# Kernel optimization log

Hardware: AMD Instinct MI355X
Metric: run time of the kernel (lower is better)

The kernel has to match this reference:

```python
import jax, jax.numpy as jnp
import numpy as np

N_PAPER, N_AUTHOR, E = 100000, 50000, 1000000
D_PAPER, D_AUTHOR, HID, OUT = 256, 128, 256, 349


def setup_inputs() -> dict:
    key = jax.random.key(0)
    ks = jax.random.split(key, 16)
    s = 0.05
    return {
        'x_paper': jax.random.normal(ks[0], (N_PAPER, D_PAPER), jnp.float32),
        'x_author': jax.random.normal(ks[1], (N_AUTHOR, D_AUTHOR), jnp.float32),
        'cites': jax.random.randint(ks[2], (2, E), 0, N_PAPER, jnp.int64 if jax.config.jax_enable_x64 else jnp.int32),
        'writes_src': jax.random.randint(ks[3], (E,), 0, N_AUTHOR),
        'writes_dst': jax.random.randint(ks[4], (E,), 0, N_PAPER),
        'gcn_W1': jax.random.normal(ks[5], (D_PAPER, HID), jnp.float32) * s,
        'gcn_b1': jnp.zeros((HID,), jnp.float32),
        'sage_Wl1': jax.random.normal(ks[6], (D_AUTHOR, HID), jnp.float32) * s,
        'sage_bl1': jnp.zeros((HID,), jnp.float32),
        'sage_Wr1': jax.random.normal(ks[7], (D_PAPER, HID), jnp.float32) * s,
        'gcn_W2': jax.random.normal(ks[8], (HID, HID), jnp.float32) * s,
        'gcn_b2': jnp.zeros((HID,), jnp.float32),
        'sage_Wl2': jax.random.normal(ks[9], (D_AUTHOR, HID), jnp.float32) * s,
        'sage_bl2': jnp.zeros((HID,), jnp.float32),
        'sage_Wr2': jax.random.normal(ks[10], (HID, HID), jnp.float32) * s,
        'lin_W': jax.random.normal(ks[11], (HID, OUT), jnp.float32) * s,
        'lin_b': jnp.zeros((OUT,), jnp.float32),
    }


def _gcn_conv(x, W, b, src, dst, n):
    # GCNConv with add_self_loops=True, symmetric normalization
    loop = jnp.arange(n, dtype=src.dtype)
    si = jnp.concatenate([src, loop])
    di = jnp.concatenate([dst, loop])
    deg = jax.ops.segment_sum(jnp.ones_like(di, x.dtype), di, n)
    dinv = jnp.where(deg > 0, jax.lax.rsqrt(jnp.maximum(deg, 1.0)), 0.0)
    norm = dinv[si] * dinv[di]  # [E+n]
    h = x @ W                   # [n, hid]
    out = jax.ops.segment_sum(h[si] * norm[:, None], di, n)
    return out + b


def _sage_conv(x_src, x_dst, Wl, bl, Wr, src, dst, n_dst):
    # SAGEConv: mean-aggregate neighbors -> lin_l, plus root lin_r (no bias)
    agg = jax.ops.segment_sum(x_src[src], dst, n_dst)
    cnt = jax.ops.segment_sum(jnp.ones_like(dst, x_src.dtype), dst, n_dst)
    mean = agg / jnp.maximum(cnt, 1.0)[:, None]
    return mean @ Wl + bl + x_dst @ Wr


def reference(x_paper, x_author, cites, writes_src, writes_dst,
              gcn_W1, gcn_b1, sage_Wl1, sage_bl1, sage_Wr1,
              gcn_W2, gcn_b2, sage_Wl2, sage_bl2, sage_Wr2,
              lin_W, lin_b):
    n = x_paper.shape[0]
    c_src, c_dst = cites[0], cites[1]
    # layer 1: HeteroConv with aggr='sum' over the two edge-type outputs
    p = jax.nn.relu(
        _gcn_conv(x_paper, gcn_W1, gcn_b1, c_src, c_dst, n)
        + _sage_conv(x_author, x_paper, sage_Wl1, sage_bl1, sage_Wr1, writes_src, writes_dst, n))
    # layer 2 (author features are never updated by these edge types)
    p = jax.nn.relu(
        _gcn_conv(p, gcn_W2, gcn_b2, c_src, c_dst, n)
        + _sage_conv(x_author, p, sage_Wl2, sage_bl2, sage_Wr2, writes_src, writes_dst, n))
    return p @ lin_W + lin_b
```

## Files before the change

### kernel.cpp

```cpp
#include <hip/hip_runtime.h>


#define DP   256
#define DA   128
#define HIDN 256
#define DOUT 349
#define NBKT 782
#define CHUNK 4096

typedef unsigned short u16;
typedef unsigned int u32;
typedef __attribute__((ext_vector_type(8))) short bf16x8;
typedef __attribute__((ext_vector_type(4))) float f32x4;

__device__ __forceinline__ u16 bf16_rn(float x) {
  union { float f; unsigned u; } v; v.f = x;
  unsigned r = v.u + 0x7FFFu + ((v.u >> 16) & 1u);
  return (u16)(r >> 16);
}
__device__ __forceinline__ float bf16f(u16 h) {
  union { float f; unsigned u; } v; v.u = ((unsigned)h) << 16; return v.f;
}
__device__ __forceinline__ unsigned pack2(float a, float b) {
  return (unsigned)bf16_rn(a) | ((unsigned)bf16_rn(b) << 16);
}

__device__ __forceinline__ void gload16(const void* g, void* lds) {
  __builtin_amdgcn_global_load_lds(
      (const __attribute__((address_space(1))) unsigned int*)g,
      (__attribute__((address_space(3))) unsigned int*)lds, 16, 0, 0);
}

#define SCAN_TPB 256
#define SCAN_VPT 8
#define SCAN_TILE 2048

__global__ void scan_local(const int* __restrict__ in, int* __restrict__ out,
                           int* __restrict__ bsum, int n) {
  __shared__ int sdata[SCAN_TPB];
  int t = threadIdx.x;
  int base = blockIdx.x * SCAN_TILE + t * SCAN_VPT;
  int v[SCAN_VPT];
  int sum = 0;
#pragma unroll
  for (int j = 0; j < SCAN_VPT; ++j) {
    int idx = base + j;
    v[j] = (idx < n) ? in[idx] : 0;
    sum += v[j];
  }
  sdata[t] = sum;
  __syncthreads();
  for (int off = 1; off < SCAN_TPB; off <<= 1) {
    int x = (t >= off) ? sdata[t - off] : 0;
    __syncthreads();
    sdata[t] += x;
    __syncthreads();
  }
  int prefix = sdata[t] - sum;
  if (t == SCAN_TPB - 1) bsum[blockIdx.x] = sdata[t];
  int run = prefix;
#pragma unroll
  for (int j = 0; j < SCAN_VPT; ++j) {
    int idx = base + j;
    if (idx < n) out[idx] = run;
    run += v[j];
  }
}

__global__ void scan_spine(int* __restrict__ bsum, int nb) {
  __shared__ int sdata[256];
  int t = threadIdx.x;
  int v = (t < nb) ? bsum[t] : 0;
  sdata[t] = v;
  __syncthreads();
  for (int off = 1; off < 256; off <<= 1) {
    int x = (t >= off) ? sdata[t - off] : 0;
    __syncthreads();
    sdata[t] += x;
    __syncthreads();
  }
  if (t < nb) bsum[t] = sdata[t] - v;
}

__global__ void scan_add(int* __restrict__ out, const int* __restrict__ bsum, int n) {
  int add = bsum[blockIdx.x];
  int base = blockIdx.x * SCAN_TILE + threadIdx.x * SCAN_VPT;
#pragma unroll
  for (int j = 0; j < SCAN_VPT; ++j) {
    int idx = base + j;
    if (idx < n) out[idx] += add;
  }
}

__global__ __launch_bounds__(256) void sort_pass1(
    const int* __restrict__ c_src, const int* __restrict__ c_dst,
    const int* __restrict__ w_srcP, const int* __restrict__ w_dstP,
    u32* __restrict__ tmp, int* __restrict__ gcount, int* __restrict__ lofs,
    int E, int nch) {
  const int cg = blockIdx.x, t = threadIdx.x;
  const int et = cg >= nch;
  const int c = cg - et * nch;
  const int* src = et ? w_srcP : c_src;
  const int* dst = et ? w_dstP : c_dst;
  __shared__ u32 cnt[NBKT];
  __shared__ u32 ofs[NBKT];
  __shared__ u32 sdata[256];
  __shared__ u32 pay[CHUNK];
  __shared__ u16 bkt[CHUNK];

  for (int i = t; i < NBKT; i += 256) cnt[i] = 0;
  __syncthreads();
  const int base = c * CHUNK;
#pragma unroll
  for (int j = 0; j < 16; ++j) {
    int i = t + j * 256, idx = base + i;
    if (idx < E) {
      u32 s = (u32)src[idx], d = (u32)dst[idx];
      pay[i] = (s << 7) | (d & 127u);
      bkt[i] = (u16)(d >> 7);
      atomicAdd(&cnt[d >> 7], 1u);
    }
  }
  __syncthreads();
  for (int i = t; i < NBKT; i += 256)
    gcount[((size_t)et * NBKT + i) * nch + c] = (int)cnt[i];
  u32 ssum = 0;
  const int b0 = t * 4;
#pragma unroll
  for (int j = 0; j < 4; ++j) {
    int i = b0 + j;
    if (i < NBKT) ssum += cnt[i];
  }
  sdata[t] = ssum;
  __syncthreads();
  for (int o = 1; o < 256; o <<= 1) {
    u32 x = (t >= o) ? sdata[t - o] : 0;
    __syncthreads();
    sdata[t] += x;
    __syncthreads();
  }
  u32 run = sdata[t] - ssum;
#pragma unroll
  for (int j = 0; j < 4; ++j) {
    int i = b0 + j;
    if (i < NBKT) { ofs[i] = run; run += cnt[i]; }
  }
  __syncthreads();
  for (int i = t; i < NBKT; i += 256) {
    lofs[((size_t)et * nch + c) * NBKT + i] = (int)ofs[i];
    cnt[i] = ofs[i];
  }
  __syncthreads();
  u32* tout = tmp + (size_t)et * nch * CHUNK + base;
#pragma unroll
  for (int j = 0; j < 16; ++j) {
    int i = t + j * 256, idx = base + i;
    if (idx < E) {
      u32 p = atomicAdd(&cnt[bkt[i]], 1u);
      tout[p] = pay[i];
    }
  }
}

#define MAXB 2560
__global__ __launch_bounds__(256) void sort_pass2(
    const u32* __restrict__ tmp, const int* __restrict__ prefix,
    const int* __restrict__ gcount, const int* __restrict__ lofs,
    int* __restrict__ cSorted, int* __restrict__ cDeg, int* __restrict__ cOff,
    int* __restrict__ wSorted, int* __restrict__ wDeg, int* __restrict__ wOff,
    float* __restrict__ dinv,
    int E, int nch, int n, int nbk) {
  const int bg = blockIdx.x, t = threadIdx.x;
  const int et = bg >= nbk;
  const int b = bg - et * nbk;
  int* outSorted = et ? wSorted : cSorted;
  int* deg = et ? wDeg : cDeg;
  int* offArr = et ? wOff : cOff;
  __shared__ u32 est[MAXB];
  __shared__ u32 outl[MAXB];
  __shared__ u32 cnt[128], ofs[128];
  __shared__ u32 sdata[256];

  const int node0 = b << 7;
  const size_t bgl = (size_t)et * NBKT + b;
  const int ebaseG = prefix[bgl * nch];
  const int eendG = (bg == 2 * nbk - 1) ? 2 * E : prefix[(bgl + 1) * nch];
  const int ebase = ebaseG - et * E;
  const int esize = (eendG - et * E) - ebase;

  const u32* tsrc = tmp + (size_t)et * nch * CHUNK;
  for (int c = t; c < nch; c += 256) {
    int g = lofs[((size_t)et * nch + c) * NBKT + b];
    int len = gcount[bgl * nch + c];
    int dp = prefix[bgl * nch + c] - ebaseG;
    for (int k = 0; k < len; ++k)
      est[dp + k] = tsrc[(size_t)c * CHUNK + g + k];
  }
  if (t < 128) cnt[t] = 0;
  __syncthreads();
  for (int i = t; i < esize; i += 256) atomicAdd(&cnt[est[i] & 127u], 1u);
  __syncthreads();
  u32 v = (t < 128) ? cnt[t] : 0;
  sdata[t] = v;
  __syncthreads();
  for (int o = 1; o < 256; o <<= 1) {
    u32 x = (t >= o) ? sdata[t - o] : 0;
    __syncthreads();
    sdata[t] += x;
    __syncthreads();
  }
  if (t < 128) ofs[t] = sdata[t] - v;
  __syncthreads();
  const int nNodes = (n - node0) < 128 ? (n - node0) : 128;
  if (t < nNodes) {
    deg[node0 + t] = (int)cnt[t];
    offArr[node0 + t] = ebase + (int)ofs[t];
    if (et == 0) dinv[node0 + t] = rsqrtf((float)(cnt[t] + 1));
  }
  __syncthreads();
  if (t < 128) cnt[t] = ofs[t];
  __syncthreads();
  for (int i = t; i < esize; i += 256) {
    u32 e = est[i];
    u32 p = atomicAdd(&cnt[e & 127u], 1u);
    outl[p] = e >> 7;
  }
  __syncthreads();
  for (int i = t; i < esize; i += 256) outSorted[ebase + i] = (int)outl[i];
}

__global__ void prep_all(
    const float* __restrict__ x_paper, const float* __restrict__ x_author,
    u16* __restrict__ xp, u16* __restrict__ xa16,
    const float* __restrict__ W1, const float* __restrict__ Wr1,
    const float* __restrict__ W2, const float* __restrict__ Wr2,
    const float* __restrict__ Wl1, const float* __restrict__ Wl2,
    const float* __restrict__ linW,
    u16* __restrict__ BtW1, u16* __restrict__ BtWr1,
    u16* __restrict__ BtW2, u16* __restrict__ BtWr2,
    u16* __restrict__ BtWl1, u16* __restrict__ BtWl2, u16* __restrict__ BtLin,
    const float* __restrict__ b1, const float* __restrict__ bl1,
    const float* __restrict__ b2, const float* __restrict__ bl2,
    const float* __restrict__ linb,
    float* __restrict__ biasR1, float* __restrict__ biasR2,
    float* __restrict__ biasLin,
    int N, int NA) {
  const int R1 = (N * 32 + 255) / 256;
  const int R2 = R1 + (NA * 16 + 255) / 256;
  const int WB = 256 * 256 / 256;
  const int LB = 256 * 128 / 256;
  const int FB = 384 * 256 / 256;
  int bid = blockIdx.x, t = threadIdx.x;

  if (bid < R1) {
    int i = bid * 256 + t;
    if (i < N * 32) {
      const float4* x4 = (const float4*)x_paper;
      float4 v0 = x4[(size_t)i * 2];
      float4 v1 = x4[(size_t)i * 2 + 1];
      uint4 O;
      O.x = pack2(v0.x, v0.y); O.y = pack2(v0.z, v0.w);
      O.z = pack2(v1.x, v1.y); O.w = pack2(v1.z, v1.w);
      ((uint4*)xp)[i] = O;
    }
    return;
  }
  if (bid < R2) {
    int i = (bid - R1) * 256 + t;
    if (i < NA * 16) {
      const float4* x4 = (const float4*)x_author;
      float4 v0 = x4[(size_t)i * 2];
      float4 v1 = x4[(size_t)i * 2 + 1];
      uint4 O;
      O.x = pack2(v0.x, v0.y); O.y = pack2(v0.z, v0.w);
      O.z = pack2(v1.x, v1.y); O.w = pack2(v1.z, v1.w);
      ((uint4*)xa16)[i] = O;
    }
    return;
  }
  int wb = bid - R2;
  const float* W; u16* Bt; int K, Nn, Npad;
  if      (wb < WB)                  { W = W1;  Bt = BtW1;  K = 256; Nn = 256; Npad = 256; }
  else if ((wb -= WB) < WB)          { W = Wr1; Bt = BtWr1; K = 256; Nn = 256; Npad = 256; }
  else if ((wb -= WB) < WB)          { W = W2;  Bt = BtW2;  K = 256; Nn = 256; Npad = 256; }
  else if ((wb -= WB) < WB)          { W = Wr2; Bt = BtWr2; K = 256; Nn = 256; Npad = 256; }
  else if ((wb -= WB) < LB)          { W = Wl1; Bt = BtWl1; K = 128; Nn = 256; Npad = 256; }
  else if ((wb -= LB) < LB)          { W = Wl2; Bt = BtWl2; K = 128; Nn = 256; Npad = 256; }
  else if ((wb -= LB) < FB)          { W = linW; Bt = BtLin; K = 256; Nn = DOUT; Npad = 384; }
  else {
    if (t < 256) {
      biasR1[t] = b1[t] + bl1[t];
      biasR2[t] = b2[t] + bl2[t];
    }
    for (int i = t; i < 384; i += 256) biasLin[i] = (i < DOUT) ? linb[i] : 0.f;
    return;
  }
  int idx = wb * 256 + t;
  int tot = Npad * K;
  if (idx >= tot) return;
  int nn = idx / K, k = idx - nn * K;
  float v = (nn < Nn) ? W[(size_t)k * Nn + nn] : 0.f;
  Bt[idx] = bf16_rn(v);
}

__device__ __forceinline__ void agg_body(
    const uint4* __restrict__ base, const float* __restrict__ dinv,
    const int* __restrict__ c_off, const int* __restrict__ c_cnt,
    const int* __restrict__ c_sorted, u16* __restrict__ xout,
    int d, int lane) {
  const int hl = lane & 31;
  const int half = lane >> 5;
  int start = c_off[d], cnt = c_cnt[d];
  float acc[8] = {};
  for (int j0 = 0; j0 < cnt; j0 += 64) {
    int nn = cnt - j0; nn = nn < 64 ? nn : 64;
    int sl = (j0 + lane < cnt) ? c_sorted[start + j0 + lane] : 0;
    int jj = 0;
    for (; jj + 8 <= nn; jj += 8) {
      int ss[4]; float dv[4]; uint4 vv[4];
#pragma unroll
      for (int u = 0; u < 4; ++u) ss[u] = __shfl(sl, jj + 2 * u + half);
#pragma unroll
      for (int u = 0; u < 4; ++u) dv[u] = dinv[ss[u]];
#pragma unroll
      for (int u = 0; u < 4; ++u) vv[u] = base[(size_t)ss[u] * 32 + hl];
#pragma unroll
      for (int u = 0; u < 4; ++u) {
        const u16* p = (const u16*)&vv[u];
#pragma unroll
        for (int e = 0; e < 8; ++e) acc[e] = fmaf(bf16f(p[e]), dv[u], acc[e]);
      }
    }
    for (; jj < nn; jj += 2) {
      int idx = jj + half;
      int s = __shfl(sl, idx < nn ? idx : jj);
      float wgt = (idx < nn) ? dinv[s] : 0.f;
      uint4 v = base[(size_t)s * 32 + hl];
      const u16* p = (const u16*)&v;
#pragma unroll
      for (int e = 0; e < 8; ++e) acc[e] = fmaf(bf16f(p[e]), wgt, acc[e]);
    }
  }
  float dd = dinv[d];
  {
    uint4 v = base[(size_t)d * 32 + hl];
    float wgt = half ? 0.f : dd;
    const u16* p = (const u16*)&v;
#pragma unroll
    for (int e = 0; e < 8; ++e) acc[e] = fmaf(bf16f(p[e]), wgt, acc[e]);
  }
  float f[8];
#pragma unroll
  for (int e = 0; e < 8; ++e) f[e] = (acc[e] + __shfl_xor(acc[e], 32)) * dd;
  if (lane < 32) {
    uint4 O;
    O.x = pack2(f[0], f[1]); O.y = pack2(f[2], f[3]);
    O.z = pack2(f[4], f[5]); O.w = pack2(f[6], f[7]);
    ((uint4*)xout)[(size_t)d * 32 + hl] = O;
  }
}

__device__ __forceinline__ void mean_body(
    const uint4* __restrict__ xa, const int* __restrict__ w_off,
    const int* __restrict__ w_cnt, const int* __restrict__ w_sorted,
    u16* __restrict__ mean, int d, int lane) {
  const int hl = lane & 15;
  const int qt = lane >> 4;
  int start = w_off[d], cnt = w_cnt[d];
  float acc[8] = {};
  for (int j0 = 0; j0 < cnt; j0 += 64) {
    int nn = cnt - j0; nn = nn < 64 ? nn : 64;
    int sl = (j0 + lane < cnt) ? w_sorted[start + j0 + lane] : 0;
    int jj = 0;
    for (; jj + 8 <= nn; jj += 8) {
      int ss[2]; uint4 vv[2];
#pragma unroll
      for (int u = 0; u < 2; ++u) ss[u] = __shfl(sl, jj + 4 * u + qt);
#pragma unroll
      for (int u = 0; u < 2; ++u) vv[u] = xa[(size_t)ss[u] * 16 + hl];
#pragma unroll
      for (int u = 0; u < 2; ++u) {
        const u16* p = (const u16*)&vv[u];
#pragma unroll
        for (int e = 0; e < 8; ++e) acc[e] += bf16f(p[e]);
      }
    }
    for (; jj < nn; jj += 4) {
      int idx = jj + qt;
      int s = __shfl(sl, idx < nn ? idx : jj);
      float wgt = (idx < nn) ? 1.f : 0.f;
      uint4 v = xa[(size_t)s * 16 + hl];
      const u16* p = (const u16*)&v;
#pragma unroll
      for (int e = 0; e < 8; ++e) acc[e] = fmaf(bf16f(p[e]), wgt, acc[e]);
    }
  }
  float inv = 1.0f / (float)((cnt > 0) ? cnt : 1);
  float f[8];
#pragma unroll
  for (int e = 0; e < 8; ++e) {
    float x = acc[e] + __shfl_xor(acc[e], 16);
    x += __shfl_xor(x, 32);
    f[e] = x * inv;
  }
  if (lane < 16) {
    uint4 O;
    O.x = pack2(f[0], f[1]); O.y = pack2(f[2], f[3]);
    O.z = pack2(f[4], f[5]); O.w = pack2(f[6], f[7]);
    ((uint4*)mean)[(size_t)d * 16 + hl] = O;
  }
}

__global__ void gather_fused(
    const u16* __restrict__ xin, const float* __restrict__ dinv,
    const int* __restrict__ c_off, const int* __restrict__ c_cnt,
    const int* __restrict__ c_sorted, u16* __restrict__ xout,
    const u16* __restrict__ xa16, const int* __restrict__ w_off,
    const int* __restrict__ w_cnt, const int* __restrict__ w_sorted,
    u16* __restrict__ mean, int n, int nbw) {
  const int lane = threadIdx.x & 63;
  if (blockIdx.x < nbw) {
    int d = ((blockIdx.x * blockDim.x) >> 6) + (threadIdx.x >> 6);
    if (d >= n) return;
    agg_body((const uint4*)xin, dinv, c_off, c_cnt, c_sorted, xout, d, lane);
  } else {
    int d = (((blockIdx.x - nbw) * blockDim.x) >> 6) + (threadIdx.x >> 6);
    if (d >= n) return;
    mean_body((const uint4*)xa16, w_off, w_cnt, w_sorted, mean, d, lane);
  }
}

__global__ void agg_gcn(const u16* __restrict__ xin, const float* __restrict__ dinv,
                        const int* __restrict__ c_off, const int* __restrict__ c_cnt,
                        const int* __restrict__ c_sorted,
                        u16* __restrict__ xout, int n) {
  int d = (blockIdx.x * blockDim.x + threadIdx.x) >> 6;
  int lane = threadIdx.x & 63;
  if (d >= n) return;
  agg_body((const uint4*)xin, dinv, c_off, c_cnt, c_sorted, xout, d, lane);
}

template <int NSEG, bool F32OUT, int NC>
__global__ __launch_bounds__(256, 4) void gemm_bf16(
    const u16* __restrict__ A0, const u16* __restrict__ A1, const u16* __restrict__ A2,
    const u16* __restrict__ B0, const u16* __restrict__ B1, const u16* __restrict__ B2,
    const float* __restrict__ bias,
    u16* __restrict__ Cp, float* __restrict__ Cf,
    int M, int N) {
  __shared__ u16 Ah[2][4096];
  __shared__ u16 Bh[2][4096];

  const int t = threadIdx.x;
  const int wid = t >> 6, lane = t & 63;
  const int wr = wid >> 1, wc = wid & 1;
  const int lrow = lane & 15, kslot = lane >> 4;
  const int jsw = kslot ^ ((lrow >> 1) & 3);

  const int nb = gridDim.x;
  const int q = nb >> 3, r = nb & 7;
  const int xcd = blockIdx.x & 7, pos = blockIdx.x >> 3;
  const int lin = (xcd < r ? xcd * (q + 1) : r * (q + 1) + (xcd - r) * q) + pos;
  const int bx = lin / NC, by = lin - bx * NC;
  const int gm = bx * 128;
  const int gn = by * 128;

  const int s_r = lane >> 2;
  const int s_j = (lane & 3) ^ ((s_r >> 1) & 3);

  f32x4 acc[4][4];
  const f32x4 z4 = {0.f, 0.f, 0.f, 0.f};
#pragma unroll
  for (int m = 0; m < 4; ++m)
#pragma unroll
    for (int n = 0; n < 4; ++n) acc[m][n] = z4;

  const int NT = (NSEG == 3) ? 20 : 8;

  auto STAGE = [&](int tt, int half) {
    const u16* A;
    const u16* B;
    int rs, k0;
    if (NSEG == 3 && tt >= 16)     { A = A2; B = B2; rs = 128; k0 = (tt - 16) * 32; }
    else if (NSEG == 3 && tt >= 8) { A = A1; B = B1; rs = 256; k0 = (tt - 8) * 32; }
    else                           { A = A0; B = B0; rs = 256; k0 = tt * 32; }
    const int c = wid * 2;
#pragma unroll
    for (int cc = 0; cc < 2; ++cc) {
      int grow = gm + (c + cc) * 16 + s_r;
      grow = grow < M ? grow : M - 1;
      gload16(A + (size_t)grow * rs + (k0 + s_j * 8), &Ah[half][(c + cc) * 512]);
      int col = gn + (c + cc) * 16 + s_r;
      gload16(B + (size_t)col * rs + (k0 + s_j * 8), &Bh[half][(c + cc) * 512]);
    }
  };

  STAGE(0, 0);
  __syncthreads();

  for (int tt = 0; tt < NT; ++tt) {
    const int half = tt & 1;
    if (tt + 1 < NT) STAGE(tt + 1, half ^ 1);

    bf16x8 ah[4];
    const int ab = (wr * 64 + lrow) * 32 + jsw * 8;
#pragma unroll
    for (int m = 0; m < 4; ++m) ah[m] = *(const bf16x8*)&Ah[half][ab + m * 512];
    const int bb = (wc * 64 + lrow) * 32 + jsw * 8;
#pragma unroll
    for (int n = 0; n < 4; ++n) {
      bf16x8 bn = *(const bf16x8*)&Bh[half][bb + n * 512];
#pragma unroll
      for (int m = 0; m < 4; ++m)
        acc[m][n] = __builtin_amdgcn_mfma_f32_16x16x32_bf16(ah[m], bn, acc[m][n], 0, 0, 0);
    }
    __syncthreads();
  }

  const int col0 = gn + wc * 64 + lrow;
  const int row00 = gm + wr * 64 + kslot * 4;
#pragma unroll
  for (int m = 0; m < 4; ++m) {
#pragma unroll
    for (int i = 0; i < 4; ++i) {
      int row = row00 + m * 16 + i;
      if (row >= M) continue;
#pragma unroll
      for (int n = 0; n < 4; ++n) {
        int col = col0 + n * 16;
        float v = acc[m][n][i] + bias[col];
        if (F32OUT) {
          if (col < N) Cf[(size_t)row * N + col] = v;
        } else {
          Cp[(size_t)row * 256 + col] = bf16_rn(fmaxf(v, 0.f));
        }
      }
    }
  }
}

static inline size_t align_up(size_t x) { return (x + 255) & ~(size_t)255; }

extern "C" void kernel_launch(void* const* d_in, const int* in_sizes, int n_in,
                              void* d_out, int out_size, void* d_ws, size_t ws_size,
                              hipStream_t stream) {
  const float* x_paper  = (const float*)d_in[0];
  const float* x_author = (const float*)d_in[1];
  const int*   cites    = (const int*)d_in[2];
  const int*   w_src    = (const int*)d_in[3];
  const int*   w_dst    = (const int*)d_in[4];
  const float* W1  = (const float*)d_in[5];
  const float* b1  = (const float*)d_in[6];
  const float* Wl1 = (const float*)d_in[7];
  const float* bl1 = (const float*)d_in[8];
  const float* Wr1 = (const float*)d_in[9];
  const float* W2  = (const float*)d_in[10];
  const float* b2  = (const float*)d_in[11];
  const float* Wl2 = (const float*)d_in[12];
  const float* bl2 = (const float*)d_in[13];
  const float* Wr2 = (const float*)d_in[14];
  const float* linW = (const float*)d_in[15];
  const float* linb = (const float*)d_in[16];
  float* out = (float*)d_out;

  const int N = in_sizes[0] / DP;
  const int NA = in_sizes[1] / DA;
  const int E = in_sizes[3];
  const int* c_src = cites;
  const int* c_dst = cites + E;

  const int NCH = (E + CHUNK - 1) / CHUNK;
  const int NB = (N + 127) >> 7;
  const int GC2 = 2 * NB * NCH;

  char* w = (char*)d_ws;
  size_t off = 0;
  auto alloc = [&](size_t bytes) -> void* {
    void* p = w + off;
    off = align_up(off + bytes);
    return p;
  };
  int* deg_c      = (int*)alloc((size_t)N * 4);
  int* cnt_w      = (int*)alloc((size_t)N * 4);
  int* cites_off  = (int*)alloc((size_t)N * 4);
  int* writes_off = (int*)alloc((size_t)N * 4);
  int* c_sorted   = (int*)alloc((size_t)E * 4);
  int* w_sorted   = (int*)alloc((size_t)E * 4);
  u32* tmpE       = (u32*)alloc((size_t)2 * NCH * CHUNK * 4);
  int* gcount     = (int*)alloc((size_t)GC2 * 4);
  int* gprefix    = (int*)alloc((size_t)GC2 * 4);
  int* lofs       = (int*)alloc((size_t)2 * NCH * NBKT * 4);
  int* bsumA      = (int*)alloc(256 * 4);
  float* dinv     = (float*)alloc((size_t)N * 4);
  u16* xa16       = (u16*)alloc((size_t)NA * DA * 2);
  u16* meanA      = (u16*)alloc((size_t)N * DA * 2);
  u16* xp         = (u16*)alloc((size_t)N * 256 * 2);
  u16* xs         = (u16*)alloc((size_t)N * 256 * 2);
  u16* pb         = (u16*)alloc((size_t)N * 256 * 2);
  const int bsW = 256 * 256, bsL = 256 * 128, bsLin = 384 * 256;
  u16* BtW1  = (u16*)alloc((size_t)bsW * 2);
  u16* BtWr1 = (u16*)alloc((size_t)bsW * 2);
  u16* BtW2  = (u16*)alloc((size_t)bsW * 2);
  u16* BtWr2 = (u16*)alloc((size_t)bsW * 2);
  u16* BtWl1 = (u16*)alloc((size_t)bsL * 2);
  u16* BtWl2 = (u16*)alloc((size_t)bsL * 2);
  u16* BtLin = (u16*)alloc((size_t)bsLin * 2);
  float* biasR1  = (float*)alloc(256 * 4);
  float* biasR2  = (float*)alloc(256 * 4);
  float* biasLin = (float*)alloc(384 * 4);
  (void)ws_size; (void)n_in; (void)out_size;

  const int nsb2 = (GC2 + SCAN_TILE - 1) / SCAN_TILE;

  sort_pass1<<<2 * NCH, 256, 0, stream>>>(c_src, c_dst, w_src, w_dst,
                                          tmpE, gcount, lofs, E, NCH);
  scan_local<<<nsb2, SCAN_TPB, 0, stream>>>(gcount, gprefix, bsumA, GC2);
  scan_spine<<<1, 256, 0, stream>>>(bsumA, nsb2);
  scan_add<<<nsb2, SCAN_TPB, 0, stream>>>(gprefix, bsumA, GC2);
  sort_pass2<<<2 * NB, 256, 0, stream>>>(tmpE, gprefix, gcount, lofs,
                                         c_sorted, deg_c, cites_off,
                                         w_sorted, cnt_w, writes_off,
                                         dinv, E, NCH, N, NB);

  {
    const int R1 = (N * 32 + 255) / 256;
    const int R2 = R1 + (NA * 16 + 255) / 256;
    const int total = R2 + 4 * 256 + 2 * 128 + 384 + 1;
    prep_all<<<total, 256, 0, stream>>>(
        x_paper, x_author, xp, xa16,
        W1, Wr1, W2, Wr2, Wl1, Wl2, linW,
        BtW1, BtWr1, BtW2, BtWr2, BtWl1, BtWl2, BtLin,
        b1, bl1, b2, bl2, linb, biasR1, biasR2, biasLin, N, NA);
  }

  const int nbWave = (N * 64 + 255) / 256;
  const int GX = (N + 127) / 128;

  gather_fused<<<2 * nbWave, 256, 0, stream>>>(
      xp, dinv, cites_off, deg_c, c_sorted, xs,
      xa16, writes_off, cnt_w, w_sorted, meanA, N, nbWave);
  gemm_bf16<3, false, 2><<<GX * 2, 256, 0, stream>>>(
      xs, xp, meanA, BtW1, BtWr1, BtWl1, biasR1, pb, nullptr, N, HIDN);
  agg_gcn<<<nbWave, 256, 0, stream>>>(pb, dinv, cites_off, deg_c, c_sorted, xs, N);
  gemm_bf16<3, false, 2><<<GX * 2, 256, 0, stream>>>(
      xs, pb, meanA, BtW2, BtWr2, BtWl2, biasR2, xp, nullptr, N, HIDN);
  gemm_bf16<1, true, 3><<<GX * 3, 256, 0, stream>>>(
      xp, nullptr, nullptr, BtLin, nullptr, nullptr, biasLin, nullptr, out, N, DOUT);
}
```

Before: 461.2 us.

## Pre-scale features by source dinv to drop per-edge dinv gathers

The source-side GCN normalization factor is folded into a second bf16 copy of the features, written in prep_all and in the layer-1 GEMM epilogue. The aggregation loop then sums pre-scaled rows and applies only the destination dinv at the end, removing one random 4-byte gather per edge. In exchange, prep and the GEMM epilogue write an extra N×256 bf16 buffer, which adds memory traffic and workspace. Scaling before rounding to bf16 also changes rounding slightly.

```diff
diff --git a/kernel.cpp b/kernel.cpp
--- a/kernel.cpp
+++ b/kernel.cpp
@@ -231,7 +231,8 @@
 
 __global__ void prep_all(
     const float* __restrict__ x_paper, const float* __restrict__ x_author,
-    u16* __restrict__ xp, u16* __restrict__ xa16,
+    const float* __restrict__ dinv,
+    u16* __restrict__ xp, u16* __restrict__ xpd, u16* __restrict__ xa16,
     const float* __restrict__ W1, const float* __restrict__ Wr1,
     const float* __restrict__ W2, const float* __restrict__ Wr2,
     const float* __restrict__ Wl1, const float* __restrict__ Wl2,
@@ -255,13 +256,18 @@
   if (bid < R1) {
     int i = bid * 256 + t;
     if (i < N * 32) {
+      int row = i >> 5;
+      float dv = dinv[row];
       const float4* x4 = (const float4*)x_paper;
       float4 v0 = x4[(size_t)i * 2];
       float4 v1 = x4[(size_t)i * 2 + 1];
-      uint4 O;
+      uint4 O, S;
       O.x = pack2(v0.x, v0.y); O.y = pack2(v0.z, v0.w);
       O.z = pack2(v1.x, v1.y); O.w = pack2(v1.z, v1.w);
+      S.x = pack2(v0.x * dv, v0.y * dv); S.y = pack2(v0.z * dv, v0.w * dv);
+      S.z = pack2(v1.x * dv, v1.y * dv); S.w = pack2(v1.z * dv, v1.w * dv);
       ((uint4*)xp)[i] = O;
+      ((uint4*)xpd)[i] = S;
     }
     return;
   }
@@ -317,38 +323,36 @@
     int sl = (j0 + lane < cnt) ? c_sorted[start + j0 + lane] : 0;
     int jj = 0;
     for (; jj + 8 <= nn; jj += 8) {
-      int ss[4]; float dv[4]; uint4 vv[4];
+      int ss[4]; uint4 vv[4];
 #pragma unroll
       for (int u = 0; u < 4; ++u) ss[u] = __shfl(sl, jj + 2 * u + half);
-#pragma unroll
-      for (int u = 0; u < 4; ++u) dv[u] = dinv[ss[u]];
 #pragma unroll
       for (int u = 0; u < 4; ++u) vv[u] = base[(size_t)ss[u] * 32 + hl];
 #pragma unroll
       for (int u = 0; u < 4; ++u) {
         const u16* p = (const u16*)&vv[u];
 #pragma unroll
-        for (int e = 0; e < 8; ++e) acc[e] = fmaf(bf16f(p[e]), dv[u], acc[e]);
+        for (int e = 0; e < 8; ++e) acc[e] += bf16f(p[e]);
       }
     }
     for (; jj < nn; jj += 2) {
       int idx = jj + half;
       int s = __shfl(sl, idx < nn ? idx : jj);
-      float wgt = (idx < nn) ? dinv[s] : 0.f;
+      float wgt = (idx < nn) ? 1.f : 0.f;
       uint4 v = base[(size_t)s * 32 + hl];
       const u16* p = (const u16*)&v;
 #pragma unroll
       for (int e = 0; e < 8; ++e) acc[e] = fmaf(bf16f(p[e]), wgt, acc[e]);
     }
   }
-  float dd = dinv[d];
   {
     uint4 v = base[(size_t)d * 32 + hl];
-    float wgt = half ? 0.f : dd;
+    float wgt = half ? 0.f : 1.f;
     const u16* p = (const u16*)&v;
 #pragma unroll
     for (int e = 0; e < 8; ++e) acc[e] = fmaf(bf16f(p[e]), wgt, acc[e]);
   }
+  float dd = dinv[d];
   float f[8];
 #pragma unroll
   for (int e = 0; e < 8; ++e) f[e] = (acc[e] + __shfl_xor(acc[e], 32)) * dd;
@@ -412,7 +416,7 @@
 }
 
 __global__ void gather_fused(
-    const u16* __restrict__ xin, const float* __restrict__ dinv,
+    const u16* __restrict__ xind, const float* __restrict__ dinv,
     const int* __restrict__ c_off, const int* __restrict__ c_cnt,
     const int* __restrict__ c_sorted, u16* __restrict__ xout,
     const u16* __restrict__ xa16, const int* __restrict__ w_off,
@@ -422,7 +426,7 @@
   if (blockIdx.x < nbw) {
     int d = ((blockIdx.x * blockDim.x) >> 6) + (threadIdx.x >> 6);
     if (d >= n) return;
-    agg_body((const uint4*)xin, dinv, c_off, c_cnt, c_sorted, xout, d, lane);
+    agg_body((const uint4*)xind, dinv, c_off, c_cnt, c_sorted, xout, d, lane);
   } else {
     int d = (((blockIdx.x - nbw) * blockDim.x) >> 6) + (threadIdx.x >> 6);
     if (d >= n) return;
@@ -430,22 +434,22 @@
   }
 }
 
-__global__ void agg_gcn(const u16* __restrict__ xin, const float* __restrict__ dinv,
+__global__ void agg_gcn(const u16* __restrict__ xind, const float* __restrict__ dinv,
                         const int* __restrict__ c_off, const int* __restrict__ c_cnt,
                         const int* __restrict__ c_sorted,
                         u16* __restrict__ xout, int n) {
   int d = (blockIdx.x * blockDim.x + threadIdx.x) >> 6;
   int lane = threadIdx.x & 63;
   if (d >= n) return;
-  agg_body((const uint4*)xin, dinv, c_off, c_cnt, c_sorted, xout, d, lane);
+  agg_body((const uint4*)xind, dinv, c_off, c_cnt, c_sorted, xout, d, lane);
 }
 
 template <int NSEG, bool F32OUT, int NC>
 __global__ __launch_bounds__(256, 4) void gemm_bf16(
     const u16* __restrict__ A0, const u16* __restrict__ A1, const u16* __restrict__ A2,
     const u16* __restrict__ B0, const u16* __restrict__ B1, const u16* __restrict__ B2,
-    const float* __restrict__ bias,
-    u16* __restrict__ Cp, float* __restrict__ Cf,
+    const float* __restrict__ bias, const float* __restrict__ dinv,
+    u16* __restrict__ Cp, u16* __restrict__ Cpd, float* __restrict__ Cf,
     int M, int N) {
   __shared__ u16 Ah[2][4096];
   __shared__ u16 Bh[2][4096];
@@ -524,6 +528,7 @@
     for (int i = 0; i < 4; ++i) {
       int row = row00 + m * 16 + i;
       if (row >= M) continue;
+      float dv = (!F32OUT && Cpd) ? dinv[row] : 0.f;
 #pragma unroll
       for (int n = 0; n < 4; ++n) {
         int col = col0 + n * 16;
@@ -531,7 +536,9 @@
         if (F32OUT) {
           if (col < N) Cf[(size_t)row * N + col] = v;
         } else {
-          Cp[(size_t)row * 256 + col] = bf16_rn(fmaxf(v, 0.f));
+          float rv = fmaxf(v, 0.f);
+          Cp[(size_t)row * 256 + col] = bf16_rn(rv);
+          if (Cpd) Cpd[(size_t)row * 256 + col] = bf16_rn(rv * dv);
         }
       }
     }
@@ -594,8 +601,10 @@
   u16* xa16       = (u16*)alloc((size_t)NA * DA * 2);
   u16* meanA      = (u16*)alloc((size_t)N * DA * 2);
   u16* xp         = (u16*)alloc((size_t)N * 256 * 2);
+  u16* xpd        = (u16*)alloc((size_t)N * 256 * 2);
   u16* xs         = (u16*)alloc((size_t)N * 256 * 2);
   u16* pb         = (u16*)alloc((size_t)N * 256 * 2);
+  u16* pbd        = (u16*)alloc((size_t)N * 256 * 2);
   const int bsW = 256 * 256, bsL = 256 * 128, bsLin = 384 * 256;
   u16* BtW1  = (u16*)alloc((size_t)bsW * 2);
   u16* BtWr1 = (u16*)alloc((size_t)bsW * 2);
@@ -626,7 +635,7 @@
     const int R2 = R1 + (NA * 16 + 255) / 256;
     const int total = R2 + 4 * 256 + 2 * 128 + 384 + 1;
     prep_all<<<total, 256, 0, stream>>>(
-        x_paper, x_author, xp, xa16,
+        x_paper, x_author, dinv, xp, xpd, xa16,
         W1, Wr1, W2, Wr2, Wl1, Wl2, linW,
         BtW1, BtWr1, BtW2, BtWr2, BtWl1, BtWl2, BtLin,
         b1, bl1, b2, bl2, linb, biasR1, biasR2, biasLin, N, NA);
@@ -636,13 +645,14 @@
   const int GX = (N + 127) / 128;
 
   gather_fused<<<2 * nbWave, 256, 0, stream>>>(
-      xp, dinv, cites_off, deg_c, c_sorted, xs,
+      xpd, dinv, cites_off, deg_c, c_sorted, xs,
       xa16, writes_off, cnt_w, w_sorted, meanA, N, nbWave);
   gemm_bf16<3, false, 2><<<GX * 2, 256, 0, stream>>>(
-      xs, xp, meanA, BtW1, BtWr1, BtWl1, biasR1, pb, nullptr, N, HIDN);
-  agg_gcn<<<nbWave, 256, 0, stream>>>(pb, dinv, cites_off, deg_c, c_sorted, xs, N);
+      xs, xp, meanA, BtW1, BtWr1, BtWl1, biasR1, dinv, pb, pbd, nullptr, N, HIDN);
+  agg_gcn<<<nbWave, 256, 0, stream>>>(pbd, dinv, cites_off, deg_c, c_sorted, xs, N);
   gemm_bf16<3, false, 2><<<GX * 2, 256, 0, stream>>>(
-      xs, pb, meanA, BtW2, BtWr2, BtWl2, biasR2, xp, nullptr, N, HIDN);
+      xs, pb, meanA, BtW2, BtWr2, BtWl2, biasR2, nullptr, xp, nullptr, nullptr, N, HIDN);
   gemm_bf16<1, true, 3><<<GX * 3, 256, 0, stream>>>(
-      xp, nullptr, nullptr, BtLin, nullptr, nullptr, biasLin, nullptr, out, N, DOUT);
-}
+      xp, nullptr, nullptr, BtLin, nullptr, nullptr, biasLin, nullptr,
+      nullptr, nullptr, out, N, DOUT);
+}
```

Result: slower. 518.7 us (+12.5%).
